# Optimization experiments

Measured on AMD Instinct MI355X. Metric: run time of the kernel, lower is better.

The kernel has to match this reference:

```python
import jax, jax.numpy as jnp
import numpy as np

N, B, E = 50000, 1, 800000
D_IN = 128      # input_size == out_size (residual)
HID = 128       # hidden_size
H = 4           # heads
C = HID // H    # per-head dim = 32
EPS = 1e-5


def setup_inputs() -> dict:
    key = jax.random.key(0)
    ks = jax.random.split(key, 16)
    s_in = 1.0 / np.sqrt(D_IN)
    s_hid = 1.0 / np.sqrt(HID)
    return {
        "x": jax.random.normal(ks[0], (N, B, D_IN), jnp.float32),
        "edge_index": jax.random.randint(ks[1], (2, E), 0, N, jnp.int64 if jax.config.jax_enable_x64 else jnp.int32),
        "edge_attr": jax.random.normal(ks[2], (E, HID), jnp.float32),
        # TransformerConv projections (weights stored torch-style [out, in])
        "Wq": jax.random.uniform(ks[3], (HID, D_IN), jnp.float32, -s_in, s_in),
        "bq": jnp.zeros((HID,), jnp.float32),
        "Wk": jax.random.uniform(ks[4], (HID, D_IN), jnp.float32, -s_in, s_in),
        "bk": jnp.zeros((HID,), jnp.float32),
        "Wv": jax.random.uniform(ks[5], (HID, D_IN), jnp.float32, -s_in, s_in),
        "bv": jnp.zeros((HID,), jnp.float32),
        "We": jax.random.uniform(ks[6], (HID, HID), jnp.float32, -s_hid, s_hid),  # lin_edge, no bias
        "Wskip": jax.random.uniform(ks[7], (HID, D_IN), jnp.float32, -s_in, s_in),
        "bskip": jnp.zeros((HID,), jnp.float32),
        "Wp": jax.random.uniform(ks[8], (HID, HID), jnp.float32, -s_hid, s_hid),   # physics_linear
        "bp": jnp.zeros((HID,), jnp.float32),
        "Wm": jax.random.uniform(ks[9], (D_IN, HID), jnp.float32, -s_hid, s_hid),  # merge_linear
        "bm": jnp.zeros((D_IN,), jnp.float32),
    }


def reference(x, edge_index, edge_attr, Wq, bq, Wk, bk, Wv, bv, We,
              Wskip, bskip, Wp, bp, Wm, bm):
    n = x.shape[0]
    src, dst = edge_index[0], edge_index[1]  # message flows src -> dst (j -> i)

    # node-wise QKV projections -> [N, B, H, C]
    q = (x @ Wq.T + bq).reshape(n, B, H, C)
    k = (x @ Wk.T + bk).reshape(n, B, H, C)
    v = (x @ Wv.T + bv).reshape(n, B, H, C)

    # edge feature projection -> [E, H, C]
    e = (edge_attr @ We.T).reshape(-1, H, C)

    # per-edge attention scores [E, B, H]
    k_j = k[src] + e[:, None]                       # [E, B, H, C]
    alpha = (q[dst] * k_j).sum(-1) / jnp.sqrt(jnp.asarray(C, x.dtype))

    # scatter-softmax over incoming edges of each dst node
    m = jax.ops.segment_max(alpha, dst, num_segments=n)      # [N, B, H]
    a = jnp.exp(alpha - m[dst])
    s = jax.ops.segment_sum(a, dst, num_segments=n)
    alpha = a / s[dst]

    # weighted scatter-add aggregation
    msg = (v[src] + e[:, None]) * alpha[..., None]           # [E, B, H, C]
    out = jax.ops.segment_sum(msg, dst, num_segments=n)      # [N, B, H, C]
    out = out.reshape(n, B, H * C)

    # root skip connection
    out = out + (x @ Wskip.T + bskip)

    # GraphResidualBlock tail
    out = jax.nn.relu(out)
    out = out @ Wp.T + bp
    # custom LayerNorm: normalize over the node dim (dim 0), weight/bias unused
    mu = out.mean(0, keepdims=True)
    sd = out.std(0, keepdims=True)
    out = (out - mu) / (sd + EPS)
    out = jax.nn.relu(out)
    out = out @ Wm.T + bm
    return out + x
```

## Files before the change

### kernel.cpp

```cpp
#include <hip/hip_runtime.h>
#include <stdint.h>

#define RS32 0.17677669529663687f
#define LDW 40

typedef short bf16x8 __attribute__((ext_vector_type(8)));
typedef float f32x4 __attribute__((ext_vector_type(4)));

__device__ __forceinline__ ushort f2bf(float f) {
  uint32_t b = __float_as_uint(f);
  b = (b + 0x7fffu + ((b >> 16) & 1u)) >> 16;
  return (ushort)b;
}
__device__ __forceinline__ float bflo(uint32_t w) { return __uint_as_float(w << 16); }
__device__ __forceinline__ float bfhi(uint32_t w) { return __uint_as_float(w & 0xffff0000u); }

__device__ __forceinline__ void stage16(ushort* hiA, ushort* loA, int r, int koff,
                                        const float* v) {
  uint32_t hu[8], lu[8];
#pragma unroll
  for (int i = 0; i < 8; ++i) {
    ushort h0 = f2bf(v[2 * i]), h1 = f2bf(v[2 * i + 1]);
    float f0 = __uint_as_float(((uint32_t)h0) << 16);
    float f1 = __uint_as_float(((uint32_t)h1) << 16);
    ushort l0 = f2bf(v[2 * i] - f0), l1 = f2bf(v[2 * i + 1] - f1);
    hu[i] = (uint32_t)h0 | ((uint32_t)h1 << 16);
    lu[i] = (uint32_t)l0 | ((uint32_t)l1 << 16);
  }
  *(uint4*)&hiA[r * LDW + koff]     = make_uint4(hu[0], hu[1], hu[2], hu[3]);
  *(uint4*)&hiA[r * LDW + koff + 8] = make_uint4(hu[4], hu[5], hu[6], hu[7]);
  *(uint4*)&loA[r * LDW + koff]     = make_uint4(lu[0], lu[1], lu[2], lu[3]);
  *(uint4*)&loA[r * LDW + koff + 8] = make_uint4(lu[4], lu[5], lu[6], lu[7]);
}

__launch_bounds__(256)
__global__ void gemm128_mfma_kernel(int mode,
                                    const float* __restrict__ A, const float* __restrict__ A2,
                                    const float* __restrict__ W, const float* __restrict__ bias,
                                    const float* __restrict__ mu, const float* __restrict__ inv,
                                    const float* __restrict__ X, float* __restrict__ out,
                                    float* __restrict__ sums, float* __restrict__ sumsq, int N)
{
  __shared__ ushort Ahi[128 * LDW], Alo[128 * LDW], Whi[128 * LDW], Wlo[128 * LDW];
  const int tid = threadIdx.x;
  const int nb = blockIdx.x * 128;
  const int lane = tid & 63, wv = tid >> 6;
  const int wr = (wv >> 1) * 64, wc = (wv & 1) * 64;
  const int fr = lane & 15, fq = lane >> 4;
  const int sr = tid >> 1, sk = (tid & 1) * 16;

  f32x4 acc[4][4];
#pragma unroll
  for (int m = 0; m < 4; ++m)
#pragma unroll
    for (int n = 0; n < 4; ++n) acc[m][n] = (f32x4)0.0f;

  for (int kc = 0; kc < 128; kc += 32) {
    float va[16], vw[16];
    {
      int gr = nb + sr;
      if (gr < N) {
#pragma unroll
        for (int i = 0; i < 4; ++i) {
          float4 v = *(const float4*)(A + (size_t)gr * 128 + kc + sk + i * 4);
          if (mode == 1) {
            float4 b = *(const float4*)(A2 + (size_t)gr * 128 + kc + sk + i * 4);
            v.x = fmaxf(v.x + b.x, 0.f); v.y = fmaxf(v.y + b.y, 0.f);
            v.z = fmaxf(v.z + b.z, 0.f); v.w = fmaxf(v.w + b.w, 0.f);
          } else if (mode == 2) {
            float4 m4 = *(const float4*)(mu + kc + sk + i * 4);
            float4 i4 = *(const float4*)(inv + kc + sk + i * 4);
            v.x = fmaxf((v.x - m4.x) * i4.x, 0.f); v.y = fmaxf((v.y - m4.y) * i4.y, 0.f);
            v.z = fmaxf((v.z - m4.z) * i4.z, 0.f); v.w = fmaxf((v.w - m4.w) * i4.w, 0.f);
          }
          va[i * 4 + 0] = v.x; va[i * 4 + 1] = v.y; va[i * 4 + 2] = v.z; va[i * 4 + 3] = v.w;
        }
      } else {
#pragma unroll
        for (int i = 0; i < 16; ++i) va[i] = 0.f;
      }
#pragma unroll
      for (int i = 0; i < 4; ++i) {
        float4 v = *(const float4*)(W + (size_t)sr * 128 + kc + sk + i * 4);
        vw[i * 4 + 0] = v.x; vw[i * 4 + 1] = v.y; vw[i * 4 + 2] = v.z; vw[i * 4 + 3] = v.w;
      }
    }
    if (kc) __syncthreads();
    stage16(Ahi, Alo, sr, sk, va);
    stage16(Whi, Wlo, sr, sk, vw);
    __syncthreads();

    bf16x8 ah[4], al[4], bh[4], bl[4];
#pragma unroll
    for (int m = 0; m < 4; ++m) {
      const int row = wr + m * 16 + fr;
      ah[m] = *(const bf16x8*)&Ahi[row * LDW + fq * 8];
      al[m] = *(const bf16x8*)&Alo[row * LDW + fq * 8];
    }
#pragma unroll
    for (int n = 0; n < 4; ++n) {
      const int col = wc + n * 16 + fr;
      bh[n] = *(const bf16x8*)&Whi[col * LDW + fq * 8];
      bl[n] = *(const bf16x8*)&Wlo[col * LDW + fq * 8];
    }
#pragma unroll
    for (int m = 0; m < 4; ++m)
#pragma unroll
      for (int n = 0; n < 4; ++n) {
        acc[m][n] = __builtin_amdgcn_mfma_f32_16x16x32_bf16(ah[m], bh[n], acc[m][n], 0, 0, 0);
        acc[m][n] = __builtin_amdgcn_mfma_f32_16x16x32_bf16(al[m], bh[n], acc[m][n], 0, 0, 0);
        acc[m][n] = __builtin_amdgcn_mfma_f32_16x16x32_bf16(ah[m], bl[n], acc[m][n], 0, 0, 0);
      }
  }

  float bcol[4];
#pragma unroll
  for (int n = 0; n < 4; ++n) bcol[n] = bias[wc + n * 16 + fr];
  float csum[4] = {0.f, 0.f, 0.f, 0.f}, csum2[4] = {0.f, 0.f, 0.f, 0.f};
#pragma unroll
  for (int m = 0; m < 4; ++m) {
    const int r0 = nb + wr + m * 16 + fq * 4;
#pragma unroll
    for (int r = 0; r < 4; ++r) {
      const int gr = r0 + r;
      if (gr < N) {
#pragma unroll
        for (int n = 0; n < 4; ++n) {
          const int c = wc + n * 16 + fr;
          float o = acc[m][n][r] + bcol[n];
          if (mode == 2) o += X[(size_t)gr * 128 + c];
          out[(size_t)gr * 128 + c] = o;
          if (mode == 1) { csum[n] += o; csum2[n] = fmaf(o, o, csum2[n]); }
        }
      }
    }
  }
  if (mode == 1) {
#pragma unroll
    for (int n = 0; n < 4; ++n) {
      csum[n] += __shfl_xor(csum[n], 16, 64);
      csum[n] += __shfl_xor(csum[n], 32, 64);
      csum2[n] += __shfl_xor(csum2[n], 16, 64);
      csum2[n] += __shfl_xor(csum2[n], 32, 64);
    }
    if (fq == 0) {
#pragma unroll
      for (int n = 0; n < 4; ++n) {
        atomicAdd(&sums[wc + n * 16 + fr], csum[n]);
        atomicAdd(&sumsq[wc + n * 16 + fr], csum2[n]);
      }
    }
  }
}

__launch_bounds__(256)
__global__ void gemmqkvs_mfma_kernel(const float* __restrict__ x,
                                     const float* __restrict__ Wq, const float* __restrict__ bq,
                                     const float* __restrict__ Wk, const float* __restrict__ bk,
                                     const float* __restrict__ Wv, const float* __restrict__ bv,
                                     const float* __restrict__ Ws, const float* __restrict__ bs,
                                     float* __restrict__ oq, float* __restrict__ os,
                                     ushort* __restrict__ kvb, int N)
{
  const float* W; const float* bias;
  if (blockIdx.y == 0)      { W = Wq; bias = bq; }
  else if (blockIdx.y == 1) { W = Wk; bias = bk; }
  else if (blockIdx.y == 2) { W = Wv; bias = bv; }
  else                      { W = Ws; bias = bs; }

  __shared__ ushort Ahi[128 * LDW], Alo[128 * LDW], Whi[128 * LDW], Wlo[128 * LDW];
  const int tid = threadIdx.x;
  const int nb = blockIdx.x * 128;
  const int lane = tid & 63, wv = tid >> 6;
  const int wr = (wv >> 1) * 64, wc = (wv & 1) * 64;
  const int fr = lane & 15, fq = lane >> 4;
  const int sr = tid >> 1, sk = (tid & 1) * 16;

  f32x4 acc[4][4];
#pragma unroll
  for (int m = 0; m < 4; ++m)
#pragma unroll
    for (int n = 0; n < 4; ++n) acc[m][n] = (f32x4)0.0f;

  for (int kc = 0; kc < 128; kc += 32) {
    float va[16], vw[16];
    {
      int gr = nb + sr;
      if (gr < N) {
#pragma unroll
        for (int i = 0; i < 4; ++i) {
          float4 v = *(const float4*)(x + (size_t)gr * 128 + kc + sk + i * 4);
          va[i * 4 + 0] = v.x; va[i * 4 + 1] = v.y; va[i * 4 + 2] = v.z; va[i * 4 + 3] = v.w;
        }
      } else {
#pragma unroll
        for (int i = 0; i < 16; ++i) va[i] = 0.f;
      }
#pragma unroll
      for (int i = 0; i < 4; ++i) {
        float4 v = *(const float4*)(W + (size_t)sr * 128 + kc + sk + i * 4);
        vw[i * 4 + 0] = v.x; vw[i * 4 + 1] = v.y; vw[i * 4 + 2] = v.z; vw[i * 4 + 3] = v.w;
      }
    }
    if (kc) __syncthreads();
    stage16(Ahi, Alo, sr, sk, va);
    stage16(Whi, Wlo, sr, sk, vw);
    __syncthreads();

    bf16x8 ah[4], al[4], bh[4], bl[4];
#pragma unroll
    for (int m = 0; m < 4; ++m) {
      const int row = wr + m * 16 + fr;
      ah[m] = *(const bf16x8*)&Ahi[row * LDW + fq * 8];
      al[m] = *(const bf16x8*)&Alo[row * LDW + fq * 8];
    }
#pragma unroll
    for (int n = 0; n < 4; ++n) {
      const int col = wc + n * 16 + fr;
      bh[n] = *(const bf16x8*)&Whi[col * LDW + fq * 8];
      bl[n] = *(const bf16x8*)&Wlo[col * LDW + fq * 8];
    }
#pragma unroll
    for (int m = 0; m < 4; ++m)
#pragma unroll
      for (int n = 0; n < 4; ++n) {
        acc[m][n] = __builtin_amdgcn_mfma_f32_16x16x32_bf16(ah[m], bh[n], acc[m][n], 0, 0, 0);
        acc[m][n] = __builtin_amdgcn_mfma_f32_16x16x32_bf16(al[m], bh[n], acc[m][n], 0, 0, 0);
        acc[m][n] = __builtin_amdgcn_mfma_f32_16x16x32_bf16(ah[m], bl[n], acc[m][n], 0, 0, 0);
      }
  }

  float bcol[4];
#pragma unroll
  for (int n = 0; n < 4; ++n) bcol[n] = bias[wc + n * 16 + fr];
  const int y = blockIdx.y;
  float* outf = (y == 0) ? oq : os;
  const int voff = (y == 2) ? 128 : 0;
#pragma unroll
  for (int m = 0; m < 4; ++m) {
    const int r0 = nb + wr + m * 16 + fq * 4;
#pragma unroll
    for (int r = 0; r < 4; ++r) {
      const int gr = r0 + r;
      if (gr < N) {
#pragma unroll
        for (int n = 0; n < 4; ++n) {
          const int c = wc + n * 16 + fr;
          float o = acc[m][n][r] + bcol[n];
          if (y == 0 || y == 3) outf[(size_t)gr * 128 + c] = o;
          else kvb[(size_t)gr * 256 + voff + c] = f2bf(o);
        }
      }
    }
  }
}

__launch_bounds__(256)
__global__ void u_kernel(const float* __restrict__ q, const float* __restrict__ We,
                         ushort* __restrict__ u, int N)
{
  __shared__ float qs[64][128];
  const int tid = threadIdx.x;
  const int nb = blockIdx.x * 64;
  for (int idx = tid; idx < 64 * 128; idx += 256) {
    int r = idx >> 7, kk = idx & 127;
    qs[r][kk] = (nb + r < N) ? q[(size_t)(nb + r) * 128 + kk] : 0.f;
  }
  __syncthreads();
  const int j = tid & 127, half = tid >> 7;
  for (int h = 0; h < 4; ++h) {
    float w[32];
#pragma unroll
    for (int c = 0; c < 32; ++c) w[c] = We[(size_t)(32 * h + c) * 128 + j];
    for (int nn = half; nn < 64; nn += 2) {
      float acc = 0.f;
#pragma unroll
      for (int c4 = 0; c4 < 32; c4 += 4) {
        float4 qq = *(const float4*)&qs[nn][32 * h + c4];
        acc = fmaf(qq.x, w[c4], acc);
        acc = fmaf(qq.y, w[c4 + 1], acc);
        acc = fmaf(qq.z, w[c4 + 2], acc);
        acc = fmaf(qq.w, w[c4 + 3], acc);
      }
      int gr = nb + nn;
      if (gr < N) u[(size_t)gr * 512 + h * 128 + j] = f2bf(acc);
    }
  }
}

__global__ void prep_web_kernel(const float* __restrict__ We, ushort* __restrict__ WeB)
{
  int idx = blockIdx.x * 256 + threadIdx.x;
  if (idx >= 128 * 512) return;
  int c = idx >> 9, j = idx & 511;
  int hh = j >> 7, k2 = j & 127;
  WeB[idx] = (hh == (c >> 5)) ? f2bf(We[(size_t)c * 128 + k2]) : (ushort)0;
}

__global__ void deg_kernel(const int* __restrict__ ei, int* __restrict__ deg, int E)
{
  int e = blockIdx.x * 256 + threadIdx.x;
  if (e < E) atomicAdd(&deg[ei[E + e]], 1);
}

__launch_bounds__(256)
__global__ void start_kernel(const int* __restrict__ deg, int* __restrict__ offs,
                             int* __restrict__ cursor, int* __restrict__ gcount, int N)
{
  const int i = blockIdx.x * 256 + threadIdx.x;
  const int lane = threadIdx.x & 63;
  int d = (i < N) ? deg[i] : 0;
  int scan = d;
#pragma unroll
  for (int ofs = 1; ofs < 64; ofs <<= 1) {
    int t = __shfl_up(scan, ofs, 64);
    if (lane >= ofs) scan += t;
  }
  int total = __shfl(scan, 63, 64);
  int base = 0;
  if (lane == 63) base = atomicAdd(gcount, total);
  base = __shfl(base, 63, 64);
  int excl = base + scan - d;
  if (i < N) { offs[i] = excl; cursor[i] = excl; }
}

__global__ void fill_kernel(const int* __restrict__ ei, int* __restrict__ cursor,
                            int2* __restrict__ csr, int E)
{
  int e = blockIdx.x * 256 + threadIdx.x;
  if (e < E) {
    int dst = ei[E + e];
    int slot = atomicAdd(&cursor[dst], 1);
    csr[slot] = make_int2(ei[e], e);
  }
}

__launch_bounds__(256)
__global__ void fused_attn2_kernel(const int2* __restrict__ csr, const int* __restrict__ offs,
                                   const int* __restrict__ deg,
                                   const float* __restrict__ q, const ushort* __restrict__ kvb,
                                   const ushort* __restrict__ u,
                                   const float* __restrict__ eattr,
                                   ushort* __restrict__ aggS, float* __restrict__ wsS, int N)
{
  const int tid = threadIdx.x;
  const int lane = tid & 63;
  const int wid = tid >> 6;
  const int p = lane >> 5;
  const int j32 = lane & 31;
  const int c0 = j32 * 4;
  const int h = j32 >> 3;
  const int gwave = blockIdx.x * 4 + wid;
  const int nwaves = gridDim.x * 4;

  for (int n = gwave; n < N; n += nwaves) {
    const int e0 = offs[n];
    const int e1 = e0 + deg[n];

    const float4 qv = *(const float4*)(q + (size_t)n * 128 + c0);
    float uh[4][4];
#pragma unroll
    for (int hh = 0; hh < 4; ++hh) {
      uint2 U = *(const uint2*)(u + (size_t)n * 512 + hh * 128 + c0);
      uh[hh][0] = bflo(U.x); uh[hh][1] = bfhi(U.x);
      uh[hh][2] = bflo(U.y); uh[hh][3] = bfhi(U.y);
    }

    float ws0 = 0.f, ws1 = 0.f, ws2 = 0.f, ws3 = 0.f;
    float ax[4][4];
#pragma unroll
    for (int hh = 0; hh < 4; ++hh)
#pragma unroll
      for (int j = 0; j < 4; ++j) ax[hh][j] = 0.f;
    float sm0 = 0.f, sm1 = 0.f, sm2 = 0.f, sm3 = 0.f;

    int sl = e0 + p;
    if (sl < e1) {
      int2 seC = csr[sl];
      float4 eaC = *(const float4*)(eattr + (size_t)seC.y * 128 + c0);
      uint2 kC = *(const uint2*)(kvb + (size_t)seC.x * 256 + c0);
      uint2 vC = *(const uint2*)(kvb + (size_t)seC.x * 256 + 128 + c0);
      int sln = sl + 2;
      int2 seN = (sln < e1) ? csr[sln] : seC;
      for (; sl < e1; sl += 2) {
        float4 eaN = *(const float4*)(eattr + (size_t)seN.y * 128 + c0);
        uint2 kN = *(const uint2*)(kvb + (size_t)seN.x * 256 + c0);
        uint2 vN = *(const uint2*)(kvb + (size_t)seN.x * 256 + 128 + c0);
        const int slf = sl + 4;
        int2 seF = (slf < e1) ? csr[slf] : seN;

        const float kf0 = bflo(kC.x), kf1 = bfhi(kC.x), kf2 = bflo(kC.y), kf3 = bfhi(kC.y);
        const float vf0 = bflo(vC.x), vf1 = bfhi(vC.x), vf2 = bflo(vC.y), vf3 = bfhi(vC.y);

        float P0 = eaC.x * uh[0][0] + eaC.y * uh[0][1] + eaC.z * uh[0][2] + eaC.w * uh[0][3];
        float P1 = eaC.x * uh[1][0] + eaC.y * uh[1][1] + eaC.z * uh[1][2] + eaC.w * uh[1][3];
        float P2 = eaC.x * uh[2][0] + eaC.y * uh[2][1] + eaC.z * uh[2][2] + eaC.w * uh[2][3];
        float P3 = eaC.x * uh[3][0] + eaC.y * uh[3][1] + eaC.z * uh[3][2] + eaC.w * uh[3][3];
        const float qk = qv.x * kf0 + qv.y * kf1 + qv.z * kf2 + qv.w * kf3;
        P0 += (h == 0) ? qk : 0.f;
        P1 += (h == 1) ? qk : 0.f;
        P2 += (h == 2) ? qk : 0.f;
        P3 += (h == 3) ? qk : 0.f;
#pragma unroll
        for (int mm = 1; mm <= 16; mm <<= 1) {
          P0 += __shfl_xor(P0, mm, 64);
          P1 += __shfl_xor(P1, mm, 64);
          P2 += __shfl_xor(P2, mm, 64);
          P3 += __shfl_xor(P3, mm, 64);
        }
        const float a0 = __expf(P0 * RS32);
        const float a1 = __expf(P1 * RS32);
        const float a2 = __expf(P2 * RS32);
        const float a3 = __expf(P3 * RS32);
        sm0 += a0; sm1 += a1; sm2 += a2; sm3 += a3;
        const float aV = (h == 0) ? a0 : (h == 1) ? a1 : (h == 2) ? a2 : a3;
        ws0 = fmaf(aV, vf0, ws0); ws1 = fmaf(aV, vf1, ws1);
        ws2 = fmaf(aV, vf2, ws2); ws3 = fmaf(aV, vf3, ws3);
        ax[0][0] = fmaf(a0, eaC.x, ax[0][0]); ax[0][1] = fmaf(a0, eaC.y, ax[0][1]);
        ax[0][2] = fmaf(a0, eaC.z, ax[0][2]); ax[0][3] = fmaf(a0, eaC.w, ax[0][3]);
        ax[1][0] = fmaf(a1, eaC.x, ax[1][0]); ax[1][1] = fmaf(a1, eaC.y, ax[1][1]);
        ax[1][2] = fmaf(a1, eaC.z, ax[1][2]); ax[1][3] = fmaf(a1, eaC.w, ax[1][3]);
        ax[2][0] = fmaf(a2, eaC.x, ax[2][0]); ax[2][1] = fmaf(a2, eaC.y, ax[2][1]);
        ax[2][2] = fmaf(a2, eaC.z, ax[2][2]); ax[2][3] = fmaf(a2, eaC.w, ax[2][3]);
        ax[3][0] = fmaf(a3, eaC.x, ax[3][0]); ax[3][1] = fmaf(a3, eaC.y, ax[3][1]);
        ax[3][2] = fmaf(a3, eaC.z, ax[3][2]); ax[3][3] = fmaf(a3, eaC.w, ax[3][3]);

        eaC = eaN; kC = kN; vC = vN; seN = seF;
      }
    }

#pragma unroll
    for (int hh = 0; hh < 4; ++hh)
#pragma unroll
      for (int j = 0; j < 4; ++j) ax[hh][j] += __shfl_xor(ax[hh][j], 32, 64);
    ws0 += __shfl_xor(ws0, 32, 64); ws1 += __shfl_xor(ws1, 32, 64);
    ws2 += __shfl_xor(ws2, 32, 64); ws3 += __shfl_xor(ws3, 32, 64);
    sm0 += __shfl_xor(sm0, 32, 64); sm1 += __shfl_xor(sm1, 32, 64);
    sm2 += __shfl_xor(sm2, 32, 64); sm3 += __shfl_xor(sm3, 32, 64);

    const float iv0 = (sm0 > 0.f) ? 1.f / sm0 : 0.f;
    const float iv1 = (sm1 > 0.f) ? 1.f / sm1 : 0.f;
    const float iv2 = (sm2 > 0.f) ? 1.f / sm2 : 0.f;
    const float iv3 = (sm3 > 0.f) ? 1.f / sm3 : 0.f;

    if (p == 0) {
      const float s = (h == 0) ? iv0 : (h == 1) ? iv1 : (h == 2) ? iv2 : iv3;
      *(float4*)(wsS + (size_t)n * 128 + c0) =
          make_float4(ws0 * s, ws1 * s, ws2 * s, ws3 * s);
    }

    float o0[4], o1[4], s0, s1;
    if (p == 0) {
#pragma unroll
      for (int j = 0; j < 4; ++j) { o0[j] = ax[0][j]; o1[j] = ax[1][j]; }
      s0 = iv0; s1 = iv1;
    } else {
#pragma unroll
      for (int j = 0; j < 4; ++j) { o0[j] = ax[2][j]; o1[j] = ax[3][j]; }
      s0 = iv2; s1 = iv3;
    }
    uint2 w0 = make_uint2(((uint32_t)f2bf(o0[0] * s0)) | (((uint32_t)f2bf(o0[1] * s0)) << 16),
                          ((uint32_t)f2bf(o0[2] * s0)) | (((uint32_t)f2bf(o0[3] * s0)) << 16));
    uint2 w1 = make_uint2(((uint32_t)f2bf(o1[0] * s1)) | (((uint32_t)f2bf(o1[1] * s1)) << 16),
                          ((uint32_t)f2bf(o1[2] * s1)) | (((uint32_t)f2bf(o1[3] * s1)) << 16));
    *(uint2*)(aggS + (size_t)n * 512 + (p * 2) * 128 + c0) = w0;
    *(uint2*)(aggS + (size_t)n * 512 + (p * 2 + 1) * 128 + c0) = w1;
  }
}

__launch_bounds__(256)
__global__ void agg_gemm_kernel(const ushort* __restrict__ aggS, const ushort* __restrict__ WeB,
                                const float* __restrict__ wsX, float* __restrict__ attn, int N)
{
  __shared__ ushort As[128][72];
  __shared__ ushort Bs[128][72];
  const int tid = threadIdx.x;
  const int nb = blockIdx.x * 128;
  const int lane = tid & 63, wv = tid >> 6;
  const int wr = (wv >> 1) * 64, wc = (wv & 1) * 64;
  const int fr = lane & 15, fq = lane >> 4;
  const int r = tid >> 1, cs = (tid & 1) * 32;

  f32x4 acc[4][4];
#pragma unroll
  for (int m = 0; m < 4; ++m)
#pragma unroll
    for (int n = 0; n < 4; ++n) acc[m][n] = (f32x4)0.0f;

  for (int kc = 0; kc < 512; kc += 64) {
    uint4 av[4], bv[4];
    if (nb + r < N) {
      const uint4* src = (const uint4*)(aggS + (size_t)(nb + r) * 512 + kc + cs);
      av[0] = src[0]; av[1] = src[1]; av[2] = src[2]; av[3] = src[3];
    } else {
#pragma unroll
      for (int i = 0; i < 4; ++i) av[i] = make_uint4(0, 0, 0, 0);
    }
    {
      const uint4* src = (const uint4*)(WeB + (size_t)r * 512 + kc + cs);
      bv[0] = src[0]; bv[1] = src[1]; bv[2] = src[2]; bv[3] = src[3];
    }
    if (kc) __syncthreads();
#pragma unroll
    for (int i = 0; i < 4; ++i) {
      *(uint4*)&As[r][cs + i * 8] = av[i];
      *(uint4*)&Bs[r][cs + i * 8] = bv[i];
    }
    __syncthreads();

#pragma unroll
    for (int s = 0; s < 2; ++s) {
      bf16x8 ah[4], bh[4];
#pragma unroll
      for (int m = 0; m < 4; ++m)
        ah[m] = *(const bf16x8*)&As[wr + m * 16 + fr][s * 32 + fq * 8];
#pragma unroll
      for (int n = 0; n < 4; ++n)
        bh[n] = *(const bf16x8*)&Bs[wc + n * 16 + fr][s * 32 + fq * 8];
#pragma unroll
      for (int m = 0; m < 4; ++m)
#pragma unroll
        for (int n = 0; n < 4; ++n)
          acc[m][n] = __builtin_amdgcn_mfma_f32_16x16x32_bf16(ah[m], bh[n], acc[m][n], 0, 0, 0);
    }
  }

#pragma unroll
  for (int m = 0; m < 4; ++m) {
    const int r0 = nb + wr + m * 16 + fq * 4;
#pragma unroll
    for (int rr = 0; rr < 4; ++rr) {
      const int gr = r0 + rr;
      if (gr < N) {
#pragma unroll
        for (int n = 0; n < 4; ++n) {
          const int c = wc + n * 16 + fr;
          attn[(size_t)gr * 128 + c] = acc[m][n][rr] + wsX[(size_t)gr * 128 + c];
        }
      }
    }
  }
}

__global__ void finalize_stats_kernel(const float* __restrict__ sums, const float* __restrict__ sumsq,
                                      float* __restrict__ mu, float* __restrict__ inv, int N)
{
  int c = threadIdx.x;
  float m = sums[c] / (float)N;
  float var = sumsq[c] / (float)N - m * m;
  float sd = sqrtf(fmaxf(var, 0.f));
  mu[c] = m;
  inv[c] = 1.f / (sd + 1e-5f);
}

extern "C" void kernel_launch(void* const* d_in, const int* in_sizes, int n_in,
                              void* d_out, int out_size, void* d_ws, size_t ws_size,
                              hipStream_t stream) {
  const float* x    = (const float*)d_in[0];
  const int*   ei   = (const int*)d_in[1];
  const float* eatt = (const float*)d_in[2];
  const float* Wq = (const float*)d_in[3];  const float* bq = (const float*)d_in[4];
  const float* Wk = (const float*)d_in[5];  const float* bk = (const float*)d_in[6];
  const float* Wv = (const float*)d_in[7];  const float* bv = (const float*)d_in[8];
  const float* We = (const float*)d_in[9];
  const float* Wsk = (const float*)d_in[10]; const float* bsk = (const float*)d_in[11];
  const float* Wp = (const float*)d_in[12]; const float* bp = (const float*)d_in[13];
  const float* Wm = (const float*)d_in[14]; const float* bm = (const float*)d_in[15];
  float* out = (float*)d_out;

  const int N = in_sizes[0] / 128;
  const int E = in_sizes[1] / 2;

  char* w = (char*)d_ws;
  auto alloc = [&](size_t bytes) {
    char* p = w;
    w += (bytes + 255) & ~(size_t)255;
    return p;
  };
  const size_t node_f = (size_t)N * 128 * sizeof(float);
  float*  q    = (float*)alloc(node_f);
  float*  skip = (float*)alloc(node_f);
  float*  wsA  = (float*)alloc(node_f);
  ushort* kvb  = (ushort*)alloc((size_t)N * 256 * sizeof(ushort));
  ushort* u    = (ushort*)alloc((size_t)N * 512 * sizeof(ushort));
  ushort* aggS = (ushort*)alloc((size_t)N * 512 * sizeof(ushort));
  ushort* WeB  = (ushort*)alloc(128 * 512 * sizeof(ushort));
  int*    deg  = (int*)alloc((size_t)N * sizeof(int));
  int*    offs = (int*)alloc((size_t)N * sizeof(int));
  int*    curs = (int*)alloc((size_t)N * sizeof(int));
  int*    gcnt = (int*)alloc(sizeof(int));
  int2*   csr  = (int2*)alloc((size_t)E * sizeof(int2));
  float*  sums  = (float*)alloc(128 * sizeof(float));
  float*  sumsq = (float*)alloc(128 * sizeof(float));
  float*  mu    = (float*)alloc(128 * sizeof(float));
  float*  inv   = (float*)alloc(128 * sizeof(float));
  float*  t1   = q;
  (void)ws_size; (void)n_in; (void)out_size;

  const int NB = (N + 127) / 128;
  const int EB = (E + 255) / 256;

  hipMemsetAsync(deg, 0, (size_t)N * sizeof(int), stream);
  hipMemsetAsync(gcnt, 0, sizeof(int), stream);
  hipMemsetAsync(sums, 0, 2 * 128 * sizeof(float), stream);

  gemmqkvs_mfma_kernel<<<dim3(NB, 4), 256, 0, stream>>>(x, Wq, bq, Wk, bk, Wv, bv, Wsk, bsk,
                                                        q, skip, kvb, N);
  u_kernel<<<(N + 63) / 64, 256, 0, stream>>>(q, We, u, N);
  prep_web_kernel<<<256, 256, 0, stream>>>(We, WeB);

  deg_kernel<<<EB, 256, 0, stream>>>(ei, deg, E);
  start_kernel<<<(N + 255) / 256, 256, 0, stream>>>(deg, offs, curs, gcnt, N);
  fill_kernel<<<EB, 256, 0, stream>>>(ei, curs, csr, E);

  fused_attn2_kernel<<<2048, 256, 0, stream>>>(csr, offs, deg, q, kvb, u, eatt,
                                               aggS, wsA, N);

  agg_gemm_kernel<<<NB, 256, 0, stream>>>(aggS, WeB, wsA, wsA, N);

  gemm128_mfma_kernel<<<NB, 256, 0, stream>>>(1, wsA, skip, Wp, bp, nullptr, nullptr, nullptr,
                                              t1, sums, sumsq, N);
  finalize_stats_kernel<<<1, 128, 0, stream>>>(sums, sumsq, mu, inv, N);

  gemm128_mfma_kernel<<<NB, 256, 0, stream>>>(2, t1, nullptr, Wm, bm, mu, inv, x, out,
                                              nullptr, nullptr, N);
}
```

Measured before the change: 512.5 us.

## Fold u projection into QKV GEMM via precomputed Wq·We weights, store q as bf16

Instead of computing q and then a separate u = q·We per head, precomputes Mt = (Wq per-head)^T·We and bu on device, and adds four extra grid rows to the QKV GEMM so u comes directly from x via MFMA. q is now written as bf16, which halves its read traffic in the attention kernel. The hi/lo split in stage16 uses truncation instead of round-to-nearest, and the attention kernel gets an occupancy launch bound. The tradeoff is more GEMM work (8 instead of 4 weight blocks) and slightly different rounding of q and u.

```diff
diff --git a/kernel.cpp b/kernel.cpp
--- a/kernel.cpp
+++ b/kernel.cpp
@@ -20,12 +20,12 @@
   uint32_t hu[8], lu[8];
 #pragma unroll
   for (int i = 0; i < 8; ++i) {
-    ushort h0 = f2bf(v[2 * i]), h1 = f2bf(v[2 * i + 1]);
-    float f0 = __uint_as_float(((uint32_t)h0) << 16);
-    float f1 = __uint_as_float(((uint32_t)h1) << 16);
-    ushort l0 = f2bf(v[2 * i] - f0), l1 = f2bf(v[2 * i + 1] - f1);
-    hu[i] = (uint32_t)h0 | ((uint32_t)h1 << 16);
-    lu[i] = (uint32_t)l0 | ((uint32_t)l1 << 16);
+    uint32_t b0 = __float_as_uint(v[2 * i]), b1 = __float_as_uint(v[2 * i + 1]);
+    uint32_t h0m = b0 & 0xffff0000u, h1m = b1 & 0xffff0000u;
+    hu[i] = (b0 >> 16) | h1m;
+    float l0 = v[2 * i] - __uint_as_float(h0m);
+    float l1 = v[2 * i + 1] - __uint_as_float(h1m);
+    lu[i] = (__float_as_uint(l0) >> 16) | (__float_as_uint(l1) & 0xffff0000u);
   }
   *(uint4*)&hiA[r * LDW + koff]     = make_uint4(hu[0], hu[1], hu[2], hu[3]);
   *(uint4*)&hiA[r * LDW + koff + 8] = make_uint4(hu[4], hu[5], hu[6], hu[7]);
@@ -154,19 +154,22 @@
 }
 
 __launch_bounds__(256)
-__global__ void gemmqkvs_mfma_kernel(const float* __restrict__ x,
-                                     const float* __restrict__ Wq, const float* __restrict__ bq,
-                                     const float* __restrict__ Wk, const float* __restrict__ bk,
-                                     const float* __restrict__ Wv, const float* __restrict__ bv,
-                                     const float* __restrict__ Ws, const float* __restrict__ bs,
-                                     float* __restrict__ oq, float* __restrict__ os,
-                                     ushort* __restrict__ kvb, int N)
-{
+__global__ void gemmqkvsu_mfma_kernel(const float* __restrict__ x,
+                                      const float* __restrict__ Wq, const float* __restrict__ bq,
+                                      const float* __restrict__ Wk, const float* __restrict__ bk,
+                                      const float* __restrict__ Wv, const float* __restrict__ bv,
+                                      const float* __restrict__ Ws, const float* __restrict__ bs,
+                                      const float* __restrict__ Mt, const float* __restrict__ bu,
+                                      float* __restrict__ os, ushort* __restrict__ kvb,
+                                      ushort* __restrict__ u, ushort* __restrict__ qb, int N)
+{
+  const int y = blockIdx.y;
   const float* W; const float* bias;
-  if (blockIdx.y == 0)      { W = Wq; bias = bq; }
-  else if (blockIdx.y == 1) { W = Wk; bias = bk; }
-  else if (blockIdx.y == 2) { W = Wv; bias = bv; }
-  else                      { W = Ws; bias = bs; }
+  if (y == 0)      { W = Wk; bias = bk; }
+  else if (y == 1) { W = Wv; bias = bv; }
+  else if (y == 2) { W = Ws; bias = bs; }
+  else if (y == 7) { W = Wq; bias = bq; }
+  else             { W = Mt + (size_t)(y - 3) * 128 * 128; bias = bu + (y - 3) * 128; }
 
   __shared__ ushort Ahi[128 * LDW], Alo[128 * LDW], Whi[128 * LDW], Wlo[128 * LDW];
   const int tid = threadIdx.x;
@@ -233,9 +236,6 @@
   float bcol[4];
 #pragma unroll
   for (int n = 0; n < 4; ++n) bcol[n] = bias[wc + n * 16 + fr];
-  const int y = blockIdx.y;
-  float* outf = (y == 0) ? oq : os;
-  const int voff = (y == 2) ? 128 : 0;
 #pragma unroll
   for (int m = 0; m < 4; ++m) {
     const int r0 = nb + wr + m * 16 + fq * 4;
@@ -247,45 +247,41 @@
         for (int n = 0; n < 4; ++n) {
           const int c = wc + n * 16 + fr;
           float o = acc[m][n][r] + bcol[n];
-          if (y == 0 || y == 3) outf[(size_t)gr * 128 + c] = o;
-          else kvb[(size_t)gr * 256 + voff + c] = f2bf(o);
+          if (y == 2)      os[(size_t)gr * 128 + c] = o;
+          else if (y == 7) qb[(size_t)gr * 128 + c] = f2bf(o);
+          else if (y == 0) kvb[(size_t)gr * 256 + c] = f2bf(o);
+          else if (y == 1) kvb[(size_t)gr * 256 + 128 + c] = f2bf(o);
+          else             u[(size_t)gr * 512 + (y - 3) * 128 + c] = f2bf(o);
         }
       }
     }
   }
 }
 
-__launch_bounds__(256)
-__global__ void u_kernel(const float* __restrict__ q, const float* __restrict__ We,
-                         ushort* __restrict__ u, int N)
-{
-  __shared__ float qs[64][128];
+__global__ void prep_mt_kernel(const float* __restrict__ Wq, const float* __restrict__ We,
+                               float* __restrict__ Mt)
+{
   const int tid = threadIdx.x;
-  const int nb = blockIdx.x * 64;
-  for (int idx = tid; idx < 64 * 128; idx += 256) {
-    int r = idx >> 7, kk = idx & 127;
-    qs[r][kk] = (nb + r < N) ? q[(size_t)(nb + r) * 128 + kk] : 0.f;
-  }
-  __syncthreads();
-  const int j = tid & 127, half = tid >> 7;
-  for (int h = 0; h < 4; ++h) {
-    float w[32];
-#pragma unroll
-    for (int c = 0; c < 32; ++c) w[c] = We[(size_t)(32 * h + c) * 128 + j];
-    for (int nn = half; nn < 64; nn += 2) {
-      float acc = 0.f;
-#pragma unroll
-      for (int c4 = 0; c4 < 32; c4 += 4) {
-        float4 qq = *(const float4*)&qs[nn][32 * h + c4];
-        acc = fmaf(qq.x, w[c4], acc);
-        acc = fmaf(qq.y, w[c4 + 1], acc);
-        acc = fmaf(qq.z, w[c4 + 2], acc);
-        acc = fmaf(qq.w, w[c4 + 3], acc);
-      }
-      int gr = nb + nn;
-      if (gr < N) u[(size_t)gr * 512 + h * 128 + j] = f2bf(acc);
-    }
-  }
+  const int jp = blockIdx.x * 2 + (tid >> 7);
+  const int d = tid & 127;
+  const int h = jp >> 7, j = jp & 127;
+  const float* wq = Wq + (size_t)(32 * h) * 128 + d;
+  const float* we = We + (size_t)(32 * h) * 128 + j;
+  float acc = 0.f;
+#pragma unroll 8
+  for (int a = 0; a < 32; ++a) acc = fmaf(wq[a * 128], we[a * 128], acc);
+  Mt[(size_t)jp * 128 + d] = acc;
+}
+
+__global__ void prep_bu_kernel(const float* __restrict__ bq, const float* __restrict__ We,
+                               float* __restrict__ bu)
+{
+  const int jp = threadIdx.x;
+  const int h = jp >> 7, j = jp & 127;
+  float acc = 0.f;
+  for (int a = 0; a < 32; ++a)
+    acc = fmaf(bq[32 * h + a], We[(size_t)(32 * h + a) * 128 + j], acc);
+  bu[jp] = acc;
 }
 
 __global__ void prep_web_kernel(const float* __restrict__ We, ushort* __restrict__ WeB)
@@ -335,10 +331,10 @@
   }
 }
 
-__launch_bounds__(256)
+__launch_bounds__(256, 8)
 __global__ void fused_attn2_kernel(const int2* __restrict__ csr, const int* __restrict__ offs,
                                    const int* __restrict__ deg,
-                                   const float* __restrict__ q, const ushort* __restrict__ kvb,
+                                   const ushort* __restrict__ qb, const ushort* __restrict__ kvb,
                                    const ushort* __restrict__ u,
                                    const float* __restrict__ eattr,
                                    ushort* __restrict__ aggS, float* __restrict__ wsS, int N)
@@ -357,14 +353,11 @@
     const int e0 = offs[n];
     const int e1 = e0 + deg[n];
 
-    const float4 qv = *(const float4*)(q + (size_t)n * 128 + c0);
-    float uh[4][4];
-#pragma unroll
-    for (int hh = 0; hh < 4; ++hh) {
-      uint2 U = *(const uint2*)(u + (size_t)n * 512 + hh * 128 + c0);
-      uh[hh][0] = bflo(U.x); uh[hh][1] = bfhi(U.x);
-      uh[hh][2] = bflo(U.y); uh[hh][3] = bfhi(U.y);
-    }
+    const uint2 qp = *(const uint2*)(qb + (size_t)n * 128 + c0);
+    uint2 uhp[4];
+#pragma unroll
+    for (int hh = 0; hh < 4; ++hh)
+      uhp[hh] = *(const uint2*)(u + (size_t)n * 512 + hh * 128 + c0);
 
     float ws0 = 0.f, ws1 = 0.f, ws2 = 0.f, ws3 = 0.f;
     float ax[4][4];
@@ -389,14 +382,16 @@
         const int slf = sl + 4;
         int2 seF = (slf < e1) ? csr[slf] : seN;
 
-        const float kf0 = bflo(kC.x), kf1 = bfhi(kC.x), kf2 = bflo(kC.y), kf3 = bfhi(kC.y);
-        const float vf0 = bflo(vC.x), vf1 = bfhi(vC.x), vf2 = bflo(vC.y), vf3 = bfhi(vC.y);
-
-        float P0 = eaC.x * uh[0][0] + eaC.y * uh[0][1] + eaC.z * uh[0][2] + eaC.w * uh[0][3];
-        float P1 = eaC.x * uh[1][0] + eaC.y * uh[1][1] + eaC.z * uh[1][2] + eaC.w * uh[1][3];
-        float P2 = eaC.x * uh[2][0] + eaC.y * uh[2][1] + eaC.z * uh[2][2] + eaC.w * uh[2][3];
-        float P3 = eaC.x * uh[3][0] + eaC.y * uh[3][1] + eaC.z * uh[3][2] + eaC.w * uh[3][3];
-        const float qk = qv.x * kf0 + qv.y * kf1 + qv.z * kf2 + qv.w * kf3;
+        float P0 = eaC.x * bflo(uhp[0].x) + eaC.y * bfhi(uhp[0].x)
+                 + eaC.z * bflo(uhp[0].y) + eaC.w * bfhi(uhp[0].y);
+        float P1 = eaC.x * bflo(uhp[1].x) + eaC.y * bfhi(uhp[1].x)
+                 + eaC.z * bflo(uhp[1].y) + eaC.w * bfhi(uhp[1].y);
+        float P2 = eaC.x * bflo(uhp[2].x) + eaC.y * bfhi(uhp[2].x)
+                 + eaC.z * bflo(uhp[2].y) + eaC.w * bfhi(uhp[2].y);
+        float P3 = eaC.x * bflo(uhp[3].x) + eaC.y * bfhi(uhp[3].x)
+                 + eaC.z * bflo(uhp[3].y) + eaC.w * bfhi(uhp[3].y);
+        const float qk = bflo(qp.x) * bflo(kC.x) + bfhi(qp.x) * bfhi(kC.x)
+                       + bflo(qp.y) * bflo(kC.y) + bfhi(qp.y) * bfhi(kC.y);
         P0 += (h == 0) ? qk : 0.f;
         P1 += (h == 1) ? qk : 0.f;
         P2 += (h == 2) ? qk : 0.f;
@@ -414,8 +409,8 @@
         const float a3 = __expf(P3 * RS32);
         sm0 += a0; sm1 += a1; sm2 += a2; sm3 += a3;
         const float aV = (h == 0) ? a0 : (h == 1) ? a1 : (h == 2) ? a2 : a3;
-        ws0 = fmaf(aV, vf0, ws0); ws1 = fmaf(aV, vf1, ws1);
-        ws2 = fmaf(aV, vf2, ws2); ws3 = fmaf(aV, vf3, ws3);
+        ws0 = fmaf(aV, bflo(vC.x), ws0); ws1 = fmaf(aV, bfhi(vC.x), ws1);
+        ws2 = fmaf(aV, bflo(vC.y), ws2); ws3 = fmaf(aV, bfhi(vC.y), ws3);
         ax[0][0] = fmaf(a0, eaC.x, ax[0][0]); ax[0][1] = fmaf(a0, eaC.y, ax[0][1]);
         ax[0][2] = fmaf(a0, eaC.z, ax[0][2]); ax[0][3] = fmaf(a0, eaC.w, ax[0][3]);
         ax[1][0] = fmaf(a1, eaC.x, ax[1][0]); ax[1][1] = fmaf(a1, eaC.y, ax[1][1]);
@@ -578,13 +573,16 @@
     return p;
   };
   const size_t node_f = (size_t)N * 128 * sizeof(float);
-  float*  q    = (float*)alloc(node_f);
   float*  skip = (float*)alloc(node_f);
   float*  wsA  = (float*)alloc(node_f);
+  float*  t1   = (float*)alloc(node_f);
+  ushort* qb   = (ushort*)alloc((size_t)N * 128 * sizeof(ushort));
   ushort* kvb  = (ushort*)alloc((size_t)N * 256 * sizeof(ushort));
   ushort* u    = (ushort*)alloc((size_t)N * 512 * sizeof(ushort));
   ushort* aggS = (ushort*)alloc((size_t)N * 512 * sizeof(ushort));
   ushort* WeB  = (ushort*)alloc(128 * 512 * sizeof(ushort));
+  float*  Mt   = (float*)alloc(512 * 128 * sizeof(float));
+  float*  bu   = (float*)alloc(512 * sizeof(float));
   int*    deg  = (int*)alloc((size_t)N * sizeof(int));
   int*    offs = (int*)alloc((size_t)N * sizeof(int));
   int*    curs = (int*)alloc((size_t)N * sizeof(int));
@@ -594,7 +592,6 @@
   float*  sumsq = (float*)alloc(128 * sizeof(float));
   float*  mu    = (float*)alloc(128 * sizeof(float));
   float*  inv   = (float*)alloc(128 * sizeof(float));
-  float*  t1   = q;
   (void)ws_size; (void)n_in; (void)out_size;
 
   const int NB = (N + 127) / 128;
@@ -604,16 +601,18 @@
   hipMemsetAsync(gcnt, 0, sizeof(int), stream);
   hipMemsetAsync(sums, 0, 2 * 128 * sizeof(float), stream);
 
-  gemmqkvs_mfma_kernel<<<dim3(NB, 4), 256, 0, stream>>>(x, Wq, bq, Wk, bk, Wv, bv, Wsk, bsk,
-                                                        q, skip, kvb, N);
-  u_kernel<<<(N + 63) / 64, 256, 0, stream>>>(q, We, u, N);
+  prep_mt_kernel<<<256, 256, 0, stream>>>(Wq, We, Mt);
+  prep_bu_kernel<<<1, 512, 0, stream>>>(bq, We, bu);
   prep_web_kernel<<<256, 256, 0, stream>>>(We, WeB);
+
+  gemmqkvsu_mfma_kernel<<<dim3(NB, 8), 256, 0, stream>>>(x, Wq, bq, Wk, bk, Wv, bv, Wsk, bsk,
+                                                         Mt, bu, skip, kvb, u, qb, N);
 
   deg_kernel<<<EB, 256, 0, stream>>>(ei, deg, E);
   start_kernel<<<(N + 255) / 256, 256, 0, stream>>>(deg, offs, curs, gcnt, N);
   fill_kernel<<<EB, 256, 0, stream>>>(ei, curs, csr, E);
 
-  fused_attn2_kernel<<<2048, 256, 0, stream>>>(csr, offs, deg, q, kvb, u, eatt,
+  fused_attn2_kernel<<<2048, 256, 0, stream>>>(csr, offs, deg, qb, kvb, u, eatt,
                                                aggS, wsA, N);
 
   agg_gemm_kernel<<<NB, 256, 0, stream>>>(aggS, WeB, wsA, wsA, N);
```

After: 792.9 us. 1.55x slower.
